# Performance work log

Hardware: AMD Instinct MI355X
Metric: run time of the kernel (lower is better)

The kernel has to match this reference:

```python
import jax, jax.numpy as jnp
import numpy as np

DIM = 1024
HDIM = 4 * DIM
E = 8        # num_routed_experts
TOP_K = 2
B, T = 2, 2048


def setup_inputs() -> dict:
    key = jax.random.key(0)
    ks = jax.random.split(key, 6)
    std = 0.5 * DIM ** -0.5  # matches original init scale
    return {
        "x": jax.random.normal(ks[0], (B, T, DIM), jnp.float32),
        "router_w": jax.random.normal(ks[1], (E, DIM), jnp.float32) * DIM ** -0.5,
        "w_shared_up": jax.random.uniform(ks[2], (DIM, HDIM), jnp.float32, -1.0, 1.0) * (3 ** 0.5 * std),
        "w_shared_down": jax.random.normal(ks[3], (DIM, HDIM), jnp.float32) * std,
        "w_routed_up": jax.random.uniform(ks[4], (E, DIM, HDIM), jnp.float32, -1.0, 1.0) * (3 ** 0.5 * std),
        "w_routed_down": jax.random.normal(ks[5], (E, DIM, HDIM), jnp.float32) * std,
    }


def reference(x, router_w, w_shared_up, w_shared_down, w_routed_up, w_routed_down):
    Bb, Tt, D = x.shape
    N = Bb * Tt
    xf = x.reshape(N, D)

    # --- routing ---
    logits = xf @ router_w.T                      # [N, E]
    probs = jax.nn.softmax(logits, axis=-1)
    topw, topi = jax.lax.top_k(probs, TOP_K)      # [N, K]
    topw = topw / jnp.sum(topw, axis=-1, keepdims=True)
    # per-token combine weights over experts (topk indices are distinct)
    comb = jnp.zeros((N, E), probs.dtype).at[jnp.arange(N)[:, None], topi].add(topw)

    # --- fused up projection: h_e = x @ W_shared_up + x @ W_routed_up[e] ---
    h_shared = xf @ w_shared_up                   # [N, H]
    h = h_shared[:, None, :] + jnp.einsum('nd,edh->neh', xf, w_routed_up)  # [N, E, H]
    h = jnp.square(jax.nn.relu(h))                # relu(h)^2

    # --- down projection: y_e = h_e @ W_shared_down.T + h_e @ W_routed_down[e].T ---
    y = jnp.einsum('neh,dh->ned', h, w_shared_down) \
        + jnp.einsum('neh,edh->ned', h, w_routed_down)  # [N, E, D]

    # --- combine (weighted scatter-add equivalent) ---
    out = jnp.einsum('ne,ned->nd', comb, y).reshape(Bb, Tt, D)

    # --- aux losses ---
    one_hot_top1 = jax.nn.one_hot(topi[:, 0], E, dtype=jnp.float32)
    tokens_per_expert = one_hot_top1.sum(axis=0)                 # [E]
    fraction_per_expert = tokens_per_expert / N
    avg_router_prob = probs.mean(axis=0)
    load_balancing_loss = E * jnp.sum(jax.lax.stop_gradient(fraction_per_expert) * avg_router_prob)
    router_z_loss = jnp.mean(jax.scipy.special.logsumexp(logits, axis=-1) ** 2)
    importance = probs.sum(axis=0)
    importance_loss = jnp.var(importance, ddof=1)  # torch.var is unbiased

    return (out, load_balancing_loss, router_z_loss, importance_loss, tokens_per_expert)
```

## Files before the change

kernel.cpp:

```cpp
#include <hip/hip_runtime.h>
#include <hip/hip_bf16.h>

#define N_TOK 4096
#define DIMD  1024
#define HDIM  4096
#define NEXP  8
#define MAXSLOT 9216
#define MAXTILE 72

typedef __attribute__((ext_vector_type(4))) float f32x4;
typedef __attribute__((ext_vector_type(8))) short bf16x8;

__device__ __forceinline__ ushort f2bf(float f) {
    __hip_bfloat16 h = __float2bfloat16(f);
    return *reinterpret_cast<ushort*>(&h);
}

__device__ __forceinline__ void async_copy16(const ushort* g, ushort* l) {
    __builtin_amdgcn_global_load_lds((const __attribute__((address_space(1))) void*)g,
                                     (__attribute__((address_space(3))) void*)l,
                                     16, 0, 0);
}

__global__ __launch_bounds__(256) void router_kernel(
    const float* __restrict__ x, const float* __restrict__ rw,
    ushort* __restrict__ xbf, int* __restrict__ tok_e, float* __restrict__ tok_w,
    float* __restrict__ aux_f, int* __restrict__ aux_i)
{
    int wave = threadIdx.x >> 6, lane = threadIdx.x & 63;
    int token = blockIdx.x * 4 + wave;
    float acc[NEXP];
#pragma unroll
    for (int e = 0; e < NEXP; ++e) acc[e] = 0.f;
    const float* xr = x + (size_t)token * DIMD;
    for (int it = 0; it < DIMD / 64; ++it) {
        int d = it * 64 + lane;
        float xv = xr[d];
        xbf[(size_t)token * DIMD + d] = f2bf(xv);
#pragma unroll
        for (int e = 0; e < NEXP; ++e) acc[e] += xv * rw[e * DIMD + d];
    }
#pragma unroll
    for (int e = 0; e < NEXP; ++e) {
        float v = acc[e];
        for (int off = 32; off; off >>= 1) v += __shfl_xor(v, off);
        acc[e] = v;
    }
    float m = acc[0];
#pragma unroll
    for (int e = 1; e < NEXP; ++e) m = fmaxf(m, acc[e]);
    float p[NEXP], s = 0.f;
#pragma unroll
    for (int e = 0; e < NEXP; ++e) { p[e] = expf(acc[e] - m); s += p[e]; }
    float lse = m + logf(s);
    float inv = 1.f / s;
    int i1 = 0; float b1 = p[0];
#pragma unroll
    for (int e = 1; e < NEXP; ++e) if (p[e] > b1) { b1 = p[e]; i1 = e; }
    int i2 = -1; float b2 = -1.f;
#pragma unroll
    for (int e = 0; e < NEXP; ++e) if (e != i1 && p[e] > b2) { b2 = p[e]; i2 = e; }
    float wsum = b1 + b2;
    float w1 = b1 / wsum, w2 = b2 / wsum;
    if (lane == 0) {
        tok_e[token * 2] = i1; tok_e[token * 2 + 1] = i2;
        tok_w[token * 2] = w1; tok_w[token * 2 + 1] = w2;
    }
    __shared__ float s_imp[NEXP]; __shared__ float s_z;
    __shared__ int s_c1[NEXP], s_c2[NEXP];
    if (threadIdx.x < NEXP) { s_imp[threadIdx.x] = 0.f; s_c1[threadIdx.x] = 0; s_c2[threadIdx.x] = 0; }
    if (threadIdx.x == 0) s_z = 0.f;
    __syncthreads();
    if (lane == 0) {
#pragma unroll
        for (int e = 0; e < NEXP; ++e) atomicAdd(&s_imp[e], p[e] * inv);
        atomicAdd(&s_z, lse * lse);
        atomicAdd(&s_c1[i1], 1);
        atomicAdd(&s_c2[i1], 1);
        atomicAdd(&s_c2[i2], 1);
    }
    __syncthreads();
    if (threadIdx.x < NEXP) {
        atomicAdd(&aux_f[threadIdx.x], s_imp[threadIdx.x]);
        atomicAdd(&aux_i[threadIdx.x], s_c1[threadIdx.x]);
        atomicAdd(&aux_i[NEXP + threadIdx.x], s_c2[threadIdx.x]);
    }
    if (threadIdx.x == 0) atomicAdd(&aux_f[NEXP], s_z);
}

__global__ void finalize_kernel(const float* __restrict__ aux_f, const int* __restrict__ aux_i,
                                float* __restrict__ out_tail, int* __restrict__ offsets,
                                int* __restrict__ cursor, int* __restrict__ tile_e)
{
    if (threadIdx.x != 0 || blockIdx.x != 0) return;
    float imp[NEXP];
    float lb = 0.f, isum = 0.f;
    for (int e = 0; e < NEXP; ++e) {
        imp[e] = aux_f[e];
        isum += imp[e];
        lb += (float)aux_i[e] * imp[e];
    }
    lb *= (float)NEXP / ((float)N_TOK * (float)N_TOK);
    float zl = aux_f[NEXP] / (float)N_TOK;
    float mean = isum / (float)NEXP;
    float var = 0.f;
    for (int e = 0; e < NEXP; ++e) { float d = imp[e] - mean; var += d * d; }
    var /= (float)(NEXP - 1);
    out_tail[0] = lb;
    out_tail[1] = zl;
    out_tail[2] = var;
    for (int e = 0; e < NEXP; ++e) out_tail[3 + e] = (float)aux_i[e];

    int off = 0;
    for (int e = 0; e < NEXP; ++e) {
        offsets[e] = off;
        off += ((aux_i[NEXP + e] + 127) >> 7) << 7;
    }
    offsets[NEXP] = off;
    int ntile = off >> 7;
    for (int tt = 0; tt < MAXTILE; ++tt) {
        int e = -1;
        if (tt < ntile) {
            for (int j = 0; j < NEXP; ++j)
                if (tt * 128 >= offsets[j] && tt * 128 < offsets[j + 1]) e = j;
        }
        tile_e[tt] = e;
    }
    for (int e = 0; e < NEXP; ++e) cursor[e] = 0;
}

__global__ void fill_kernel(const int* __restrict__ tok_e, const float* __restrict__ tok_w,
                            const int* __restrict__ offsets, int* __restrict__ cursor,
                            int* __restrict__ slot_token, float* __restrict__ slot_wt)
{
    int t = blockIdx.x * 256 + threadIdx.x;
    if (t >= N_TOK) return;
    for (int k = 0; k < 2; ++k) {
        int e = tok_e[t * 2 + k];
        int pos = atomicAdd(&cursor[e], 1);
        int slot = offsets[e] + pos;
        slot_token[slot] = t;
        slot_wt[slot] = tok_w[t * 2 + k];
    }
}

__global__ __launch_bounds__(256) void convert_up(const float* __restrict__ wsu,
                                                  const float* __restrict__ wru,
                                                  ushort* __restrict__ wup)
{
    int e = blockIdx.z;
    int h0 = blockIdx.x * 64, d0 = blockIdx.y * 64;
    __shared__ float tile[64][65];
    int c = threadIdx.x & 63, r4 = threadIdx.x >> 6;
#pragma unroll
    for (int it = 0; it < 16; ++it) {
        int r = it * 4 + r4;
        size_t gi = ((size_t)(d0 + r)) * HDIM + h0 + c;
        tile[r][c] = wsu[gi] + wru[(size_t)e * DIMD * HDIM + gi];
    }
    __syncthreads();
    int c4 = threadIdx.x & 15, rr = threadIdx.x >> 4;
#pragma unroll
    for (int it = 0; it < 4; ++it) {
        int hr = it * 16 + rr;
        ushort4 o;
        o.x = f2bf(tile[c4 * 4 + 0][hr]);
        o.y = f2bf(tile[c4 * 4 + 1][hr]);
        o.z = f2bf(tile[c4 * 4 + 2][hr]);
        o.w = f2bf(tile[c4 * 4 + 3][hr]);
        *(ushort4*)(wup + ((size_t)e * HDIM + h0 + hr) * DIMD + d0 + c4 * 4) = o;
    }
}

__global__ void convert_dn(const float* __restrict__ wsd, const float* __restrict__ wrd,
                           ushort* __restrict__ wdn)
{
    size_t i = ((size_t)blockIdx.x * 256 + threadIdx.x) * 4;
    float4 a = *(const float4*)(wrd + i);
    float4 b = *(const float4*)(wsd + (i & (size_t)0x3FFFFF));
    ushort4 o;
    o.x = f2bf(a.x + b.x); o.y = f2bf(a.y + b.y);
    o.z = f2bf(a.z + b.z); o.w = f2bf(a.w + b.w);
    *(ushort4*)(wdn + i) = o;
}

__global__ __launch_bounds__(256) void up_gemm(
    const ushort* __restrict__ xbf, const ushort* __restrict__ wup,
    const int* __restrict__ slot_token, const int* __restrict__ tile_e,
    ushort* __restrict__ hbf)
{
    int bt = blockIdx.y;
    int e = tile_e[bt];
    if (e < 0) return;
    int h0 = blockIdx.x * 128;
    __shared__ ushort As[128 * 64];
    __shared__ ushort Bs[128 * 64];
    int t = threadIdx.x;
    int wave = t >> 6, lane = t & 63;
    int s8 = lane & 7, r8 = lane >> 3;
    int p = s8 ^ r8;
    const ushort* wb = wup + ((size_t)e * HDIM + h0) * DIMD;
    const ushort* aptr[4];
    const ushort* bptr[4];
#pragma unroll
    for (int cc = 0; cc < 4; ++cc) {
        int row = wave * 32 + cc * 8 + r8;
        int tok = slot_token[bt * 128 + row];
        if (tok < 0) tok = 0;
        aptr[cc] = xbf + (size_t)tok * DIMD + p * 8;
        bptr[cc] = wb + (size_t)row * DIMD + p * 8;
    }
    ushort* lA = As + wave * 4 * 512;
    ushort* lB = Bs + wave * 4 * 512;
    int wm = (wave >> 1) << 6, wn = (wave & 1) << 6;
    int l15 = lane & 15, q = lane >> 4;
    int r7 = l15 & 7;
    f32x4 acc[4][4] = {};
    for (int k0 = 0; k0 < DIMD; k0 += 64) {
        __syncthreads();
#pragma unroll
        for (int cc = 0; cc < 4; ++cc) {
            async_copy16(aptr[cc] + k0, lA + cc * 512);
            async_copy16(bptr[cc] + k0, lB + cc * 512);
        }
        __syncthreads();
#pragma unroll
        for (int kk = 0; kk < 64; kk += 32) {
            int pr = (kk >> 3) + q;
            int so = ((pr ^ r7) << 3);
            bf16x8 a[4], b[4];
#pragma unroll
            for (int i = 0; i < 4; ++i) a[i] = *(const bf16x8*)(As + (wm + i * 16 + l15) * 64 + so);
#pragma unroll
            for (int j = 0; j < 4; ++j) b[j] = *(const bf16x8*)(Bs + (wn + j * 16 + l15) * 64 + so);
#pragma unroll
            for (int i = 0; i < 4; ++i)
#pragma unroll
                for (int j = 0; j < 4; ++j)
                    acc[i][j] = __builtin_amdgcn_mfma_f32_16x16x32_bf16(a[i], b[j], acc[i][j], 0, 0, 0);
        }
    }
    size_t rowbase = (size_t)bt * 128;
#pragma unroll
    for (int i = 0; i < 4; ++i) {
        int row = wm + i * 16 + q * 4;
#pragma unroll
        for (int r = 0; r < 4; ++r) {
            size_t rb = (rowbase + row + r) * HDIM + h0;
#pragma unroll
            for (int j = 0; j < 4; ++j) {
                float v = acc[i][j][r];
                v = fmaxf(v, 0.f); v = v * v;
                hbf[rb + wn + j * 16 + l15] = f2bf(v);
            }
        }
    }
}

__global__ __launch_bounds__(256) void down_gemm(
    const ushort* __restrict__ hbf, const ushort* __restrict__ wdn,
    const int* __restrict__ slot_token, const float* __restrict__ slot_wt,
    const int* __restrict__ tile_e, float* __restrict__ out)
{
    int bt = blockIdx.y;
    int e = tile_e[bt];
    if (e < 0) return;
    int d0 = blockIdx.x * 128;
    int kbase = blockIdx.z * (HDIM / 2);
    __shared__ ushort As[128 * 64];
    __shared__ ushort Bs[128 * 64];
    __shared__ int stok[128];
    __shared__ float swt[128];
    int t = threadIdx.x;
    if (t < 128) { stok[t] = slot_token[bt * 128 + t]; swt[t] = slot_wt[bt * 128 + t]; }
    int wave = t >> 6, lane = t & 63;
    int s8 = lane & 7, r8 = lane >> 3;
    int p = s8 ^ r8;
    const ushort* aptr[4];
    const ushort* bptr[4];
#pragma unroll
    for (int cc = 0; cc < 4; ++cc) {
        int row = wave * 32 + cc * 8 + r8;
        aptr[cc] = hbf + ((size_t)bt * 128 + row) * HDIM + p * 8;
        bptr[cc] = wdn + ((size_t)e * DIMD + d0 + row) * HDIM + p * 8;
    }
    ushort* lA = As + wave * 4 * 512;
    ushort* lB = Bs + wave * 4 * 512;
    int wm = (wave >> 1) << 6, wn = (wave & 1) << 6;
    int l15 = lane & 15, q = lane >> 4;
    int r7 = l15 & 7;
    f32x4 acc[4][4] = {};
    for (int k0 = kbase; k0 < kbase + HDIM / 2; k0 += 64) {
        __syncthreads();
#pragma unroll
        for (int cc = 0; cc < 4; ++cc) {
            async_copy16(aptr[cc] + k0, lA + cc * 512);
            async_copy16(bptr[cc] + k0, lB + cc * 512);
        }
        __syncthreads();
#pragma unroll
        for (int kk = 0; kk < 64; kk += 32) {
            int pr = (kk >> 3) + q;
            int so = ((pr ^ r7) << 3);
            bf16x8 a[4], b[4];
#pragma unroll
            for (int i = 0; i < 4; ++i) a[i] = *(const bf16x8*)(As + (wm + i * 16 + l15) * 64 + so);
#pragma unroll
            for (int j = 0; j < 4; ++j) b[j] = *(const bf16x8*)(Bs + (wn + j * 16 + l15) * 64 + so);
#pragma unroll
            for (int i = 0; i < 4; ++i)
#pragma unroll
                for (int j = 0; j < 4; ++j)
                    acc[i][j] = __builtin_amdgcn_mfma_f32_16x16x32_bf16(a[i], b[j], acc[i][j], 0, 0, 0);
        }
    }
#pragma unroll
    for (int i = 0; i < 4; ++i) {
#pragma unroll
        for (int r = 0; r < 4; ++r) {
            int row = wm + i * 16 + q * 4 + r;
            int tok = stok[row];
            if (tok < 0) continue;
            float wgt = swt[row];
            float* orow = out + (size_t)tok * DIMD + d0 + wn;
#pragma unroll
            for (int j = 0; j < 4; ++j)
                atomicAdd(orow + j * 16 + l15, wgt * acc[i][j][r]);
        }
    }
}

extern "C" void kernel_launch(void* const* d_in, const int* in_sizes, int n_in,
                              void* d_out, int out_size, void* d_ws, size_t ws_size,
                              hipStream_t stream)
{
    const float* x   = (const float*)d_in[0];
    const float* rw  = (const float*)d_in[1];
    const float* wsu = (const float*)d_in[2];
    const float* wsd = (const float*)d_in[3];
    const float* wru = (const float*)d_in[4];
    const float* wrd = (const float*)d_in[5];
    float* out = (float*)d_out;

    char* ws = (char*)d_ws;
    size_t off = 0;
    auto alloc = [&](size_t b) { size_t o = off; off = (off + b + 255) & ~(size_t)255; return o; };
    float* aux_f     = (float*)(ws + alloc(16 * 4));
    int*   aux_i     = (int*)(ws + alloc(16 * 4));
    int*   tok_e     = (int*)(ws + alloc(N_TOK * 2 * 4));
    float* tok_w     = (float*)(ws + alloc(N_TOK * 2 * 4));
    int*   offsets   = (int*)(ws + alloc(16 * 4));
    int*   cursor    = (int*)(ws + alloc(8 * 4));
    int*   tile_e    = (int*)(ws + alloc(128 * 4));
    int*   slot_token= (int*)(ws + alloc(MAXSLOT * 4));
    float* slot_wt   = (float*)(ws + alloc(MAXSLOT * 4));
    ushort* xbf      = (ushort*)(ws + alloc((size_t)N_TOK * DIMD * 2));
    ushort* wup      = (ushort*)(ws + alloc((size_t)NEXP * HDIM * DIMD * 2));
    ushort* wdn      = (ushort*)(ws + alloc((size_t)NEXP * DIMD * HDIM * 2));
    ushort* hbf      = (ushort*)(ws + alloc((size_t)MAXSLOT * HDIM * 2));
    (void)ws_size; (void)in_sizes; (void)n_in;

    hipMemsetAsync(d_out, 0, (size_t)out_size * 4, stream);
    hipMemsetAsync(aux_f, 0, 16 * 4, stream);
    hipMemsetAsync(aux_i, 0, 16 * 4, stream);
    hipMemsetAsync(slot_token, 0xFF, MAXSLOT * 4, stream);

    router_kernel<<<N_TOK / 4, 256, 0, stream>>>(x, rw, xbf, tok_e, tok_w, aux_f, aux_i);
    finalize_kernel<<<1, 64, 0, stream>>>(aux_f, aux_i, out + (size_t)N_TOK * DIMD,
                                          offsets, cursor, tile_e);
    fill_kernel<<<N_TOK / 256, 256, 0, stream>>>(tok_e, tok_w, offsets, cursor, slot_token, slot_wt);
    convert_up<<<dim3(HDIM / 64, DIMD / 64, NEXP), 256, 0, stream>>>(wsu, wru, wup);
    convert_dn<<<(NEXP * DIMD * HDIM) / (256 * 4), 256, 0, stream>>>(wsd, wrd, wdn);
    up_gemm<<<dim3(HDIM / 128, MAXTILE), 256, 0, stream>>>(xbf, wup, slot_token, tile_e, hbf);
    down_gemm<<<dim3(DIMD / 128, MAXTILE, 2), 256, 0, stream>>>(hbf, wdn, slot_token, slot_wt, tile_e, out);
}
```

Baseline: 697.5 us.

## Enlarge GEMM row tiles to 256 and reuse shared weight tile across experts

Expert padding and tile granularity change from 128 to 256 rows, and both grouped GEMMs now compute 256x128 output tiles, with each wave owning 64 rows by 128 columns (4x8 MFMA accumulators). This raises arithmetic intensity per loaded weight tile and halves the number of row tiles. convert_up now loads the shared up-weight tile once and loops over all 8 experts, avoiding 8 redundant reads of w_shared_up. The costs are more padding waste per expert, larger register and LDS use (launch bounds request 2 blocks per SM), and fewer blocks to fill the GPU.

```diff
diff --git a/kernel.cpp b/kernel.cpp
--- a/kernel.cpp
+++ b/kernel.cpp
@@ -5,8 +5,8 @@
 #define DIMD  1024
 #define HDIM  4096
 #define NEXP  8
-#define MAXSLOT 9216
-#define MAXTILE 72
+#define MAXSLOT 10240
+#define MAXTILE 40
 
 typedef __attribute__((ext_vector_type(4))) float f32x4;
 typedef __attribute__((ext_vector_type(8))) short bf16x8;
@@ -114,15 +114,15 @@
     int off = 0;
     for (int e = 0; e < NEXP; ++e) {
         offsets[e] = off;
-        off += ((aux_i[NEXP + e] + 127) >> 7) << 7;
+        off += ((aux_i[NEXP + e] + 255) >> 8) << 8;
     }
     offsets[NEXP] = off;
-    int ntile = off >> 7;
+    int ntile = off >> 8;
     for (int tt = 0; tt < MAXTILE; ++tt) {
         int e = -1;
         if (tt < ntile) {
             for (int j = 0; j < NEXP; ++j)
-                if (tt * 128 >= offsets[j] && tt * 128 < offsets[j + 1]) e = j;
+                if (tt * 256 >= offsets[j] && tt * 256 < offsets[j + 1]) e = j;
         }
         tile_e[tt] = e;
     }
@@ -148,27 +148,34 @@
                                                   const float* __restrict__ wru,
                                                   ushort* __restrict__ wup)
 {
-    int e = blockIdx.z;
     int h0 = blockIdx.x * 64, d0 = blockIdx.y * 64;
-    __shared__ float tile[64][65];
+    __shared__ float tS[64][65];
+    __shared__ float tR[64][65];
     int c = threadIdx.x & 63, r4 = threadIdx.x >> 6;
 #pragma unroll
     for (int it = 0; it < 16; ++it) {
         int r = it * 4 + r4;
-        size_t gi = ((size_t)(d0 + r)) * HDIM + h0 + c;
-        tile[r][c] = wsu[gi] + wru[(size_t)e * DIMD * HDIM + gi];
-    }
-    __syncthreads();
+        tS[r][c] = wsu[((size_t)(d0 + r)) * HDIM + h0 + c];
+    }
     int c4 = threadIdx.x & 15, rr = threadIdx.x >> 4;
-#pragma unroll
-    for (int it = 0; it < 4; ++it) {
-        int hr = it * 16 + rr;
-        ushort4 o;
-        o.x = f2bf(tile[c4 * 4 + 0][hr]);
-        o.y = f2bf(tile[c4 * 4 + 1][hr]);
-        o.z = f2bf(tile[c4 * 4 + 2][hr]);
-        o.w = f2bf(tile[c4 * 4 + 3][hr]);
-        *(ushort4*)(wup + ((size_t)e * HDIM + h0 + hr) * DIMD + d0 + c4 * 4) = o;
+    for (int e = 0; e < NEXP; ++e) {
+        __syncthreads();
+#pragma unroll
+        for (int it = 0; it < 16; ++it) {
+            int r = it * 4 + r4;
+            tR[r][c] = wru[(size_t)e * DIMD * HDIM + ((size_t)(d0 + r)) * HDIM + h0 + c];
+        }
+        __syncthreads();
+#pragma unroll
+        for (int it = 0; it < 4; ++it) {
+            int hr = it * 16 + rr;
+            ushort4 o;
+            o.x = f2bf(tS[c4 * 4 + 0][hr] + tR[c4 * 4 + 0][hr]);
+            o.y = f2bf(tS[c4 * 4 + 1][hr] + tR[c4 * 4 + 1][hr]);
+            o.z = f2bf(tS[c4 * 4 + 2][hr] + tR[c4 * 4 + 2][hr]);
+            o.w = f2bf(tS[c4 * 4 + 3][hr] + tR[c4 * 4 + 3][hr]);
+            *(ushort4*)(wup + ((size_t)e * HDIM + h0 + hr) * DIMD + d0 + c4 * 4) = o;
+        }
     }
 }
 
@@ -184,7 +191,7 @@
     *(ushort4*)(wdn + i) = o;
 }
 
-__global__ __launch_bounds__(256) void up_gemm(
+__global__ __launch_bounds__(256, 2) void up_gemm(
     const ushort* __restrict__ xbf, const ushort* __restrict__ wup,
     const int* __restrict__ slot_token, const int* __restrict__ tile_e,
     ushort* __restrict__ hbf)
@@ -193,71 +200,71 @@
     int e = tile_e[bt];
     if (e < 0) return;
     int h0 = blockIdx.x * 128;
-    __shared__ ushort As[128 * 64];
+    __shared__ ushort As[256 * 64];
     __shared__ ushort Bs[128 * 64];
-    int t = threadIdx.x;
-    int wave = t >> 6, lane = t & 63;
+    int t = threadIdx.x, wave = t >> 6, lane = t & 63;
     int s8 = lane & 7, r8 = lane >> 3;
     int p = s8 ^ r8;
     const ushort* wb = wup + ((size_t)e * HDIM + h0) * DIMD;
-    const ushort* aptr[4];
+    const ushort* aptr[8];
     const ushort* bptr[4];
 #pragma unroll
-    for (int cc = 0; cc < 4; ++cc) {
-        int row = wave * 32 + cc * 8 + r8;
-        int tok = slot_token[bt * 128 + row];
+    for (int c = 0; c < 8; ++c) {
+        int row = wave * 64 + c * 8 + r8;
+        int tok = slot_token[bt * 256 + row];
         if (tok < 0) tok = 0;
-        aptr[cc] = xbf + (size_t)tok * DIMD + p * 8;
-        bptr[cc] = wb + (size_t)row * DIMD + p * 8;
-    }
-    ushort* lA = As + wave * 4 * 512;
-    ushort* lB = Bs + wave * 4 * 512;
-    int wm = (wave >> 1) << 6, wn = (wave & 1) << 6;
-    int l15 = lane & 15, q = lane >> 4;
-    int r7 = l15 & 7;
-    f32x4 acc[4][4] = {};
+        aptr[c] = xbf + (size_t)tok * DIMD + p * 8;
+    }
+#pragma unroll
+    for (int c = 0; c < 4; ++c) {
+        int row = wave * 32 + c * 8 + r8;
+        bptr[c] = wb + (size_t)row * DIMD + p * 8;
+    }
+    ushort* lA = As + wave * 64 * 64;
+    ushort* lB = Bs + wave * 32 * 64;
+    int wm = wave * 64;
+    int l15 = lane & 15, q = lane >> 4, r7 = l15 & 7;
+    f32x4 acc[4][8] = {};
     for (int k0 = 0; k0 < DIMD; k0 += 64) {
         __syncthreads();
 #pragma unroll
-        for (int cc = 0; cc < 4; ++cc) {
-            async_copy16(aptr[cc] + k0, lA + cc * 512);
-            async_copy16(bptr[cc] + k0, lB + cc * 512);
-        }
+        for (int c = 0; c < 8; ++c) async_copy16(aptr[c] + k0, lA + c * 512);
+#pragma unroll
+        for (int c = 0; c < 4; ++c) async_copy16(bptr[c] + k0, lB + c * 512);
         __syncthreads();
 #pragma unroll
         for (int kk = 0; kk < 64; kk += 32) {
             int pr = (kk >> 3) + q;
             int so = ((pr ^ r7) << 3);
-            bf16x8 a[4], b[4];
+            bf16x8 a[4], b[8];
 #pragma unroll
             for (int i = 0; i < 4; ++i) a[i] = *(const bf16x8*)(As + (wm + i * 16 + l15) * 64 + so);
 #pragma unroll
-            for (int j = 0; j < 4; ++j) b[j] = *(const bf16x8*)(Bs + (wn + j * 16 + l15) * 64 + so);
+            for (int j = 0; j < 8; ++j) b[j] = *(const bf16x8*)(Bs + (j * 16 + l15) * 64 + so);
 #pragma unroll
             for (int i = 0; i < 4; ++i)
 #pragma unroll
-                for (int j = 0; j < 4; ++j)
+                for (int j = 0; j < 8; ++j)
                     acc[i][j] = __builtin_amdgcn_mfma_f32_16x16x32_bf16(a[i], b[j], acc[i][j], 0, 0, 0);
         }
     }
-    size_t rowbase = (size_t)bt * 128;
+    size_t rowbase = (size_t)bt * 256;
 #pragma unroll
     for (int i = 0; i < 4; ++i) {
-        int row = wm + i * 16 + q * 4;
 #pragma unroll
         for (int r = 0; r < 4; ++r) {
-            size_t rb = (rowbase + row + r) * HDIM + h0;
-#pragma unroll
-            for (int j = 0; j < 4; ++j) {
+            size_t rb = (rowbase + wm + i * 16 + q * 4 + r) * HDIM + h0;
+#pragma unroll
+            for (int j = 0; j < 8; ++j) {
                 float v = acc[i][j][r];
                 v = fmaxf(v, 0.f); v = v * v;
-                hbf[rb + wn + j * 16 + l15] = f2bf(v);
+                hbf[rb + j * 16 + l15] = f2bf(v);
             }
         }
     }
 }
 
-__global__ __launch_bounds__(256) void down_gemm(
+__global__ __launch_bounds__(256, 2) void down_gemm(
     const ushort* __restrict__ hbf, const ushort* __restrict__ wdn,
     const int* __restrict__ slot_token, const float* __restrict__ slot_wt,
     const int* __restrict__ tile_e, float* __restrict__ out)
@@ -267,50 +274,52 @@
     if (e < 0) return;
     int d0 = blockIdx.x * 128;
     int kbase = blockIdx.z * (HDIM / 2);
-    __shared__ ushort As[128 * 64];
+    __shared__ ushort As[256 * 64];
     __shared__ ushort Bs[128 * 64];
-    __shared__ int stok[128];
-    __shared__ float swt[128];
-    int t = threadIdx.x;
-    if (t < 128) { stok[t] = slot_token[bt * 128 + t]; swt[t] = slot_wt[bt * 128 + t]; }
-    int wave = t >> 6, lane = t & 63;
+    __shared__ int stok[256];
+    __shared__ float swt[256];
+    int t = threadIdx.x, wave = t >> 6, lane = t & 63;
+    stok[t] = slot_token[bt * 256 + t];
+    swt[t]  = slot_wt[bt * 256 + t];
     int s8 = lane & 7, r8 = lane >> 3;
     int p = s8 ^ r8;
-    const ushort* aptr[4];
+    const ushort* aptr[8];
     const ushort* bptr[4];
 #pragma unroll
-    for (int cc = 0; cc < 4; ++cc) {
-        int row = wave * 32 + cc * 8 + r8;
-        aptr[cc] = hbf + ((size_t)bt * 128 + row) * HDIM + p * 8;
-        bptr[cc] = wdn + ((size_t)e * DIMD + d0 + row) * HDIM + p * 8;
-    }
-    ushort* lA = As + wave * 4 * 512;
-    ushort* lB = Bs + wave * 4 * 512;
-    int wm = (wave >> 1) << 6, wn = (wave & 1) << 6;
-    int l15 = lane & 15, q = lane >> 4;
-    int r7 = l15 & 7;
-    f32x4 acc[4][4] = {};
+    for (int c = 0; c < 8; ++c) {
+        int row = wave * 64 + c * 8 + r8;
+        aptr[c] = hbf + ((size_t)bt * 256 + row) * HDIM + p * 8;
+    }
+#pragma unroll
+    for (int c = 0; c < 4; ++c) {
+        int row = wave * 32 + c * 8 + r8;
+        bptr[c] = wdn + ((size_t)e * DIMD + d0 + row) * HDIM + p * 8;
+    }
+    ushort* lA = As + wave * 64 * 64;
+    ushort* lB = Bs + wave * 32 * 64;
+    int wm = wave * 64;
+    int l15 = lane & 15, q = lane >> 4, r7 = l15 & 7;
+    f32x4 acc[4][8] = {};
     for (int k0 = kbase; k0 < kbase + HDIM / 2; k0 += 64) {
         __syncthreads();
 #pragma unroll
-        for (int cc = 0; cc < 4; ++cc) {
-            async_copy16(aptr[cc] + k0, lA + cc * 512);
-            async_copy16(bptr[cc] + k0, lB + cc * 512);
-        }
+        for (int c = 0; c < 8; ++c) async_copy16(aptr[c] + k0, lA + c * 512);
+#pragma unroll
+        for (int c = 0; c < 4; ++c) async_copy16(bptr[c] + k0, lB + c * 512);
         __syncthreads();
 #pragma unroll
         for (int kk = 0; kk < 64; kk += 32) {
             int pr = (kk >> 3) + q;
             int so = ((pr ^ r7) << 3);
-            bf16x8 a[4], b[4];
+            bf16x8 a[4], b[8];
 #pragma unroll
             for (int i = 0; i < 4; ++i) a[i] = *(const bf16x8*)(As + (wm + i * 16 + l15) * 64 + so);
 #pragma unroll
-            for (int j = 0; j < 4; ++j) b[j] = *(const bf16x8*)(Bs + (wn + j * 16 + l15) * 64 + so);
+            for (int j = 0; j < 8; ++j) b[j] = *(const bf16x8*)(Bs + (j * 16 + l15) * 64 + so);
 #pragma unroll
             for (int i = 0; i < 4; ++i)
 #pragma unroll
-                for (int j = 0; j < 4; ++j)
+                for (int j = 0; j < 8; ++j)
                     acc[i][j] = __builtin_amdgcn_mfma_f32_16x16x32_bf16(a[i], b[j], acc[i][j], 0, 0, 0);
         }
     }
@@ -322,9 +331,9 @@
             int tok = stok[row];
             if (tok < 0) continue;
             float wgt = swt[row];
-            float* orow = out + (size_t)tok * DIMD + d0 + wn;
-#pragma unroll
-            for (int j = 0; j < 4; ++j)
+            float* orow = out + (size_t)tok * DIMD + d0;
+#pragma unroll
+            for (int j = 0; j < 8; ++j)
                 atomicAdd(orow + j * 16 + l15, wgt * acc[i][j][r]);
         }
     }
@@ -369,7 +378,7 @@
     finalize_kernel<<<1, 64, 0, stream>>>(aux_f, aux_i, out + (size_t)N_TOK * DIMD,
                                           offsets, cursor, tile_e);
     fill_kernel<<<N_TOK / 256, 256, 0, stream>>>(tok_e, tok_w, offsets, cursor, slot_token, slot_wt);
-    convert_up<<<dim3(HDIM / 64, DIMD / 64, NEXP), 256, 0, stream>>>(wsu, wru, wup);
+    convert_up<<<dim3(HDIM / 64, DIMD / 64), 256, 0, stream>>>(wsu, wru, wup);
     convert_dn<<<(NEXP * DIMD * HDIM) / (256 * 4), 256, 0, stream>>>(wsd, wrd, wdn);
     up_gemm<<<dim3(HDIM / 128, MAXTILE), 256, 0, stream>>>(xbf, wup, slot_token, tile_e, hbf);
     down_gemm<<<dim3(DIMD / 128, MAXTILE, 2), 256, 0, stream>>>(hbf, wdn, slot_token, slot_wt, tile_e, out);
```

Measured after the change: 673.7 us. 1.04x faster.
